# Kernel optimization log

Measured on AMD Instinct MI355X. Metric: run time of the kernel, lower is better.

## Reference

```python
import jax, jax.numpy as jnp
import numpy as np

B, N, DIM = 2, 128, 128
H, DH = 8, 32
DI = H * DH          # dim_inner = 256
DM = 2 * DI          # mlp_expansion_factor * dim_inner = 512
MAXDEG = 2
S = 1 + MAXDEG + MAXDEG  # 5
M1, M2 = 3, 5        # 2l+1 for degrees 1,2


def setup_inputs() -> dict:
    key = jax.random.key(0)
    ks = jax.random.split(key, 24)
    rn = lambda k, shp, sc=1.0: jax.random.normal(k, shp, jnp.float32) * sc
    s_d = DIM ** -0.5
    s_m = DM ** -0.5
    s_i = DI ** -0.5
    return {
        "h":    rn(ks[0], (B, N, DIM)),
        "t_ij": rn(ks[1], (B, N, N, DIM)),
        "r1":   rn(ks[2], (B, N, N, M1)),
        "r2":   rn(ks[3], (B, N, N, M2)),
        "x1":   rn(ks[4], (B, N, DIM, M1)),
        "x2":   rn(ks[5], (B, N, DIM, M2)),
        # LayerNorm gains (bias=False)
        "g_hi": jnp.ones((DIM,), jnp.float32),
        "g_hj": jnp.ones((DIM,), jnp.float32),
        # projections (stored as [in, out])
        "Wq":  rn(ks[6],  (DIM, DI), s_d),
        "Wk":  rn(ks[7],  (DIM, DI), s_d),
        "Wv1": rn(ks[8],  (DIM, DM), s_d), "bv1": jnp.zeros((DM,), jnp.float32),
        "Wv2": rn(ks[9],  (DM, S * DI), s_m), "bv2": jnp.zeros((S * DI,), jnp.float32),
        "Wpv1": rn(ks[10], (DIM, DM), s_d), "bpv1": jnp.zeros((DM,), jnp.float32),
        "Wpv2": rn(ks[11], (DM, S * DI), s_m), "bpv2": jnp.zeros((S * DI,), jnp.float32),
        "Wek": rn(ks[12], (DIM, S * DI), s_d),
        "Wev": rn(ks[13], (DIM, S * DI), s_d),
        "Wg":  rn(ks[14], (DIM, H * S), s_d), "bg": jnp.zeros((H * S,), jnp.float32),
        "Wo":  rn(ks[15], (DI, DIM), s_i),
    }


def _ln(x, g):
    mu = x.mean(-1, keepdims=True)
    var = ((x - mu) ** 2).mean(-1, keepdims=True)
    return (x - mu) / jnp.sqrt(var + 1e-5) * g


def reference(h, t_ij, r1, r2, x1, x2, g_hi, g_hj, Wq, Wk, Wv1, bv1, Wv2, bv2,
              Wpv1, bpv1, Wpv2, bpv2, Wek, Wev, Wg, bg, Wo):
    silu = jax.nn.silu
    hi = _ln(h, g_hi)  # b n d
    hj = _ln(h, g_hj)
    # queries/keys: b h n dh
    q = (hi @ Wq).reshape(B, N, H, DH).transpose(0, 2, 1, 3)
    k = (hj @ Wk).reshape(B, N, H, DH).transpose(0, 2, 1, 3)
    # node values / post-attn values: b h n s dh
    v  = (silu(hj @ Wv1 + bv1) @ Wv2 + bv2).reshape(B, N, S, H, DH).transpose(0, 3, 1, 2, 4)
    pv = (silu(hj @ Wpv1 + bpv1) @ Wpv2 + bpv2).reshape(B, N, S, H, DH).transpose(0, 3, 1, 2, 4)
    # edge keys/values: b h i j s dh
    ek = silu(t_ij @ Wek).reshape(B, N, N, S, H, DH).transpose(0, 4, 1, 2, 3, 5)
    ev = (t_ij @ Wev).reshape(B, N, N, S, H, DH).transpose(0, 4, 1, 2, 3, 5)
    # keys elementwise-conditioned by edge keys, then score over dh
    sim = jnp.einsum('bhid,bhjd,bhijsd->bhijs', q, k, ek)
    attn = jax.nn.softmax(sim, axis=3)  # softmax over j (dim=-2 of b h i j s)
    # sea_ij: b h i j s dh
    sea = attn[..., None] * v[:, :, None] + ev * pv[:, :, None]
    # gates: b h i 1 s 1
    gates = jax.nn.sigmoid(hi @ Wg + bg).reshape(B, N, H, S).transpose(0, 2, 1, 3)
    out = sea * gates[:, :, :, None, :, None]
    # merge heads -> b i j s (h dh), combine -> b i j s dim
    out = out.transpose(0, 2, 3, 4, 1, 5).reshape(B, N, N, S, DI) @ Wo
    # split along s: (1, maxdeg, maxdeg) = (h_scales, r_scales, x_scales)
    h_out = h + out[..., 0, :].sum(axis=2)  # sum over j
    x1_out = (jnp.einsum('bjdm,bijd->bidm', x1, out[..., 3, :])
              + jnp.einsum('bijm,bijd->bidm', r1, out[..., 1, :]))
    x2_out = (jnp.einsum('bjdm,bijd->bidm', x2, out[..., 4, :])
              + jnp.einsum('bijm,bijd->bidm', r2, out[..., 2, :]))
    return (h_out, x1_out, x2_out)
```

## Files before the change

### kernel.cpp

```cpp
#include <hip/hip_runtime.h>
#include <math.h>

#define BB 2
#define NN 128
#define DD 128
#define DI 256
#define DM 512
#define SS 5
#define SDI 1280
#define HS 40
#define M1 3
#define M2 5

typedef __attribute__((ext_vector_type(8))) short bf16x8_t;
typedef __attribute__((ext_vector_type(4))) float f32x4_t;
typedef __attribute__((ext_vector_type(4))) float f32x4v;

#define MFMA __builtin_amdgcn_mfma_f32_16x16x32_bf16

__device__ __forceinline__ float sigm(float x){ return __fdividef(1.0f, 1.0f + __expf(-x)); }
__device__ __forceinline__ unsigned short f2bf(float f){
    union { float f; unsigned u; } v; v.f = f;
    unsigned r = v.u + 0x7FFFu + ((v.u>>16)&1u);
    return (unsigned short)(r>>16);
}
__device__ __forceinline__ unsigned pk2(float a, float b){
    return (unsigned)f2bf(a) | ((unsigned)f2bf(b)<<16);
}
__device__ __forceinline__ float bflo(unsigned u){ union{unsigned u; float f;} v; v.u = u<<16; return v.f; }
__device__ __forceinline__ float bfhi(unsigned u){ union{unsigned u; float f;} v; v.u = u & 0xFFFF0000u; return v.f; }

__global__ __launch_bounds__(256) void prep(
    const float* __restrict__ h,
    const float* __restrict__ g_hi, const float* __restrict__ g_hj,
    const float* __restrict__ Wq, const float* __restrict__ Wk,
    const float* __restrict__ Wv1, const float* __restrict__ Wpv1,
    const float* __restrict__ Wg,
    const float* __restrict__ Wek, const float* __restrict__ Wev,
    const float* __restrict__ Wo, const float* __restrict__ Wv2,
    const float* __restrict__ Wpv2,
    const float* __restrict__ x1, const float* __restrict__ x2,
    unsigned short* __restrict__ hi_ws, unsigned short* __restrict__ hj_ws,
    unsigned short* __restrict__ WekT, unsigned short* __restrict__ WevT,
    unsigned short* __restrict__ WoT, unsigned short* __restrict__ W2T,
    unsigned short* __restrict__ WnT,
    float* __restrict__ x1T, float* __restrict__ x2T)
{
    const int bx = blockIdx.x, tid = threadIdx.x;
    __shared__ unsigned short sLT[64*65];
    if (bx < 408){
        const float* src; unsigned short* dst; int W, ldD, R0, C0;
        int t = bx;
        if (t < 160){ src=Wv2;  dst=W2T;            W=SDI; ldD=DM;  R0=(t%20)*64; C0=(t/20)*64; }
        else if (t < 320){ t-=160; src=Wpv2; dst=W2T + SDI*DM; W=SDI; ldD=DM; R0=(t%20)*64; C0=(t/20)*64; }
        else if (t < 360){ t-=320; src=Wek; dst=WekT; W=SDI; ldD=DD; R0=(t%20)*64; C0=(t/20)*64; }
        else if (t < 400){ t-=360; src=Wev; dst=WevT; W=SDI; ldD=DD; R0=(t%20)*64; C0=(t/20)*64; }
        else { t-=400; src=Wo; dst=WoT; W=DD; ldD=DI; R0=(t%2)*64; C0=(t/2)*64; }
        const int tx = tid & 63, ty = tid >> 6;
        #pragma unroll
        for (int k=0;k<16;++k){
            int c = C0 + 4*k + ty;
            sLT[tx*65 + 4*k + ty] = f2bf(src[(size_t)c*W + R0 + tx]);
        }
        __syncthreads();
        #pragma unroll
        for (int k=0;k<16;++k){
            int rr = 4*k + ty;
            dst[(size_t)(R0+rr)*ldD + C0 + tx] = sLT[rr*65 + tx];
        }
    } else if (bx < 664){
        const int node = bx - 408;
        if (tid < 64){
            float h0 = h[node*DD + tid], h1 = h[node*DD + 64 + tid];
            float s1 = h0 + h1, s2 = h0*h0 + h1*h1;
            #pragma unroll
            for (int off=32; off; off>>=1){ s1 += __shfl_xor(s1,off); s2 += __shfl_xor(s2,off); }
            float mu   = s1*(1.0f/DD);
            float var  = s2*(1.0f/DD) - mu*mu;
            float rstd = rsqrtf(var + 1e-5f);
            float c0 = (h0-mu)*rstd, c1 = (h1-mu)*rstd;
            hi_ws[node*DD + tid]      = f2bf(c0*g_hi[tid]);
            hi_ws[node*DD + 64 + tid] = f2bf(c1*g_hi[64+tid]);
            hj_ws[node*DD + tid]      = f2bf(c0*g_hj[tid]);
            hj_ws[node*DD + 64 + tid] = f2bf(c1*g_hj[64+tid]);
        }
        for (int f = node*256 + tid; f < 1584*DD; f += 256*256){
            int row = f >> 7, d = f & 127;
            float v;
            if (row < 256)       v = Wq[d*DI + row];
            else if (row < 304){ int c = row-256; v = (c < HS) ? Wg[d*HS + c] : 0.0f; }
            else if (row < 560)  v = Wk[d*DI + (row-304)];
            else if (row < 1072) v = Wv1[d*DM + (row-560)];
            else                 v = Wpv1[d*DM + (row-1072)];
            WnT[f] = f2bf(v);
        }
    } else {
        const int t = bx - 664;
        const int bb = t >> 7, j = t & 127;
        const int d = tid & 127, half = tid >> 7;
        if (half == 0){
            #pragma unroll
            for (int m=0;m<M1;++m)
                x1T[((size_t)(bb*M1+m)*NN + j)*DD + d] =
                    x1[(((size_t)bb*NN + j)*DD + d)*M1 + m];
        } else {
            #pragma unroll
            for (int m=0;m<M2;++m)
                x2T[((size_t)(bb*M2+m)*NN + j)*DD + d] =
                    x2[(((size_t)bb*NN + j)*DD + d)*M2 + m];
        }
    }
}

__global__ __launch_bounds__(256,4) void node_gemm(
    const unsigned short* __restrict__ WnT,
    const unsigned short* __restrict__ hi_ws, const unsigned short* __restrict__ hj_ws,
    const float* __restrict__ bg, const float* __restrict__ bv1, const float* __restrict__ bpv1,
    float* __restrict__ q_ws, float* __restrict__ k_ws,
    float* __restrict__ g_ws, unsigned short* __restrict__ hid_ws)
{
    const int bx = blockIdx.x;
    const int tile = bx % 99, nq = bx / 99;
    const int tid = threadIdx.x, lane = tid&63, w = tid>>6;
    const int l15 = lane&15, g4 = lane>>4;
    const int ntile = nq*4 + w;
    const unsigned short* A  = WnT + (size_t)(tile*16 + l15)*DD + 8*g4;
    const unsigned short* Bp = ((tile < 19) ? hi_ws : hj_ws) + (size_t)(ntile*16 + l15)*DD + 8*g4;
    f32x4_t c = {0.f,0.f,0.f,0.f};
    #pragma unroll
    for (int ks=0; ks<4; ++ks)
        c = MFMA(*(const bf16x8_t*)(A + 32*ks), *(const bf16x8_t*)(Bp + 32*ks), c, 0,0,0);
    const int node = ntile*16 + l15;
    const int col0 = tile*16 + 4*g4;
    if (tile < 16){
        f32x4_t* dst = (f32x4_t*)(q_ws + (size_t)node*DI + col0);
        *dst = c;
    } else if (tile < 19){
        #pragma unroll
        for (int r=0;r<4;++r){
            int cc = col0 + r - 256;
            if (cc < HS) g_ws[node*HS + cc] = sigm(c[r] + bg[cc]);
        }
    } else if (tile < 35){
        f32x4_t* dst = (f32x4_t*)(k_ws + (size_t)node*DI + (col0-304));
        *dst = c;
    } else if (tile < 67){
        int cc = col0 - 560;
        float s0 = c[0]+bv1[cc], s1 = c[1]+bv1[cc+1], s2 = c[2]+bv1[cc+2], s3 = c[3]+bv1[cc+3];
        s0 *= sigm(s0); s1 *= sigm(s1); s2 *= sigm(s2); s3 *= sigm(s3);
        uint2 pkk; pkk.x = pk2(s0,s1); pkk.y = pk2(s2,s3);
        *(uint2*)(hid_ws + (size_t)node*1024 + cc) = pkk;
    } else {
        int cc = col0 - 1072;
        float s0 = c[0]+bpv1[cc], s1 = c[1]+bpv1[cc+1], s2 = c[2]+bpv1[cc+2], s3 = c[3]+bpv1[cc+3];
        s0 *= sigm(s0); s1 *= sigm(s1); s2 *= sigm(s2); s3 *= sigm(s3);
        uint2 pkk; pkk.x = pk2(s0,s1); pkk.y = pk2(s2,s3);
        *(uint2*)(hid_ws + (size_t)node*1024 + 512 + cc) = pkk;
    }
}

__global__ __launch_bounds__(256,4) void v2_gemm(
    const unsigned short* __restrict__ W2T,
    const unsigned short* __restrict__ hid_ws,
    const float* __restrict__ bv2, const float* __restrict__ bpv2,
    unsigned short* __restrict__ vpv_ws)
{
    const int bx = blockIdx.x;
    const int otile = bx % 160, nq = bx / 160;
    const int tid = threadIdx.x, lane = tid&63, w = tid>>6;
    const int l15 = lane&15, g4 = lane>>4;
    const int ntile = nq*4 + w;
    const int obase = otile*16;
    const int koff = (obase < SDI) ? 0 : 512;
    const unsigned short* A  = W2T + (size_t)(obase + l15)*DM + 8*g4;
    const unsigned short* Bp = hid_ws + (size_t)(ntile*16 + l15)*1024 + koff + 8*g4;
    f32x4_t c = {0.f,0.f,0.f,0.f};
    #pragma unroll
    for (int ks=0; ks<16; ++ks)
        c = MFMA(*(const bf16x8_t*)(A + 32*ks), *(const bf16x8_t*)(Bp + 32*ks), c, 0,0,0);
    const int node = ntile*16 + l15;
    const int o0 = obase + 4*g4;
    const float* bias = (obase < SDI) ? bv2 : bpv2;
    const int ob = (obase < SDI) ? o0 : (o0 - SDI);
    float v0 = c[0]+bias[ob], v1 = c[1]+bias[ob+1], v2 = c[2]+bias[ob+2], v3 = c[3]+bias[ob+3];
    uint2 pkk; pkk.x = pk2(v0,v1); pkk.y = pk2(v2,v3);
    *(uint2*)(vpv_ws + (size_t)node*2560 + o0) = pkk;
}

#define SH_T   0
#define SH_QK  16384
#define SH_SIM 49152
#define SH_Q   59392

__global__ __launch_bounds__(512,4) void simh(
    const float* __restrict__ t_ij,
    const unsigned short* __restrict__ WekT,
    const float* __restrict__ q_ws, const float* __restrict__ k_ws,
    float* __restrict__ sim_ws)
{
    __shared__ __align__(16) char sm[60416];
    float* sSIM = (float*)(sm + SH_SIM);
    float* sQf  = (float*)(sm + SH_Q);

    const int bx0 = blockIdx.x;
    const int bx = ((bx0 & 7) << 6) | (bx0 >> 3);
    const int node = bx >> 1, jh = bx & 1;
    const int b = node >> 7;
    const int j0 = jh*64;
    const int tid = threadIdx.x, lane = tid&63, w = tid>>6;
    const int l15 = lane&15, g4 = lane>>4;

    if (tid < DI) sQf[tid] = q_ws[(size_t)node*DI + tid];
    {
        const int j = tid>>3, seg = tid&7;
        const float* src = t_ij + (size_t)(node*NN + j0 + j)*DD + seg*16;
        char* row = sm + SH_T + j*256;
        const int swz = (j&7)<<4;
        #pragma unroll
        for (int u=0;u<4;++u){
            f32x4v tv = __builtin_nontemporal_load((const f32x4v*)(src + 4*u));
            uint2 pkk; pkk.x = pk2(tv[0],tv[1]); pkk.y = pk2(tv[2],tv[3]);
            *(uint2*)(row + ((2*(seg*16+4*u)) ^ swz)) = pkk;
        }
    }
    __syncthreads();
    {
        const int j = tid>>3, seg = tid&7;
        const float* kr = k_ws + (size_t)(b*NN + j0 + j)*DI + seg*32;
        char* row = sm + SH_QK + j*512;
        const int swz = (j&7)<<4;
        #pragma unroll
        for (int u=0;u<8;++u){
            float4 kv = *(const float4*)(kr + 4*u);
            const float* qv = sQf + seg*32 + 4*u;
            uint2 pkk; pkk.x = pk2(kv.x*qv[0], kv.y*qv[1]); pkk.y = pk2(kv.z*qv[2], kv.w*qv[3]);
            *(uint2*)(row + ((2*(seg*32+4*u)) ^ swz)) = pkk;
        }
    }
    bf16x8_t bT[4][4];
    #pragma unroll
    for (int jt=0;jt<4;++jt){
        const int jc = jt*16 + l15;
        const char* row = sm + SH_T + jc*256;
        const int swz = (jc&7)<<4;
        #pragma unroll
        for (int ks=0;ks<4;++ks)
            bT[jt][ks] = *(const bf16x8_t*)(row + ((2*(32*ks+8*g4)) ^ swz));
    }
    __syncthreads();

    for (int p5=0; p5<5; ++p5){
        const int p = w + 8*p5;
        const unsigned short* ap = WekT + (size_t)(2*p)*16*DD + (size_t)l15*DD + 8*g4;
        bf16x8_t a0[4], a1[4];
        #pragma unroll
        for (int ks=0;ks<4;++ks){
            a0[ks] = *(const bf16x8_t*)(ap + 32*ks);
            a1[ks] = *(const bf16x8_t*)(ap + 16*DD + 32*ks);
        }
        const int hs = w*SS + p5;
        const int o0 = 32*p + 4*g4;
        const int qk0 = o0 & 255;
        #pragma unroll
        for (int jt=0;jt<4;++jt){
            f32x4_t c0 = {0.f,0.f,0.f,0.f}, c1 = {0.f,0.f,0.f,0.f};
            #pragma unroll
            for (int ks=0;ks<4;++ks){
                c0 = MFMA(a0[ks], bT[jt][ks], c0, 0,0,0);
                c1 = MFMA(a1[ks], bT[jt][ks], c1, 0,0,0);
            }
            const int jr = jt*16 + l15;
            const char* qrow = sm + SH_QK + jr*512;
            const int swz = (jr&7)<<4;
            uint2 u0 = *(const uint2*)(qrow + ((2*qk0) ^ swz));
            uint2 u1 = *(const uint2*)(qrow + ((2*(qk0+16)) ^ swz));
            float part =
                (c0[0]*sigm(c0[0]))*bflo(u0.x) + (c0[1]*sigm(c0[1]))*bfhi(u0.x)
              + (c0[2]*sigm(c0[2]))*bflo(u0.y) + (c0[3]*sigm(c0[3]))*bfhi(u0.y)
              + (c1[0]*sigm(c1[0]))*bflo(u1.x) + (c1[1]*sigm(c1[1]))*bfhi(u1.x)
              + (c1[2]*sigm(c1[2]))*bflo(u1.y) + (c1[3]*sigm(c1[3]))*bfhi(u1.y);
            part += __shfl_xor(part, 16);
            part += __shfl_xor(part, 32);
            if (g4 == 0) sSIM[jr*HS + hs] = part;
        }
    }
    __syncthreads();
    {
        float* dst = sim_ws + (size_t)node*NN*HS + j0*HS;
        for (int t2=tid; t2<64*HS; t2+=512) dst[t2] = sSIM[t2];
    }
}

__global__ __launch_bounds__(256) void softmax_k(
    float* __restrict__ sim_ws, const float* __restrict__ g_ws)
{
    const int node = blockIdx.x;
    const int tid = threadIdx.x, lane = tid&63, w = tid>>6;
    float* srow = sim_ws + (size_t)node*NN*HS;
    #pragma unroll
    for (int u=0; u<10; ++u){
        const int hs = w*10 + u;
        const float gt = g_ws[node*HS + hs];
        float v0 = srow[lane*HS + hs];
        float v1 = srow[(lane+64)*HS + hs];
        float m = fmaxf(v0,v1);
        #pragma unroll
        for (int off=32; off; off>>=1) m = fmaxf(m, __shfl_xor(m,off));
        float e0 = __expf(v0-m), e1 = __expf(v1-m);
        float ssum = e0+e1;
        #pragma unroll
        for (int off=32; off; off>>=1) ssum += __shfl_xor(ssum,off);
        float inv = __fdividef(gt, ssum);
        srow[lane*HS + hs]      = e0*inv;
        srow[(lane+64)*HS + hs] = e1*inv;
    }
}

#define EV_BODY(S, ATTIDX, EPILOG)                                                \
    _Pragma("unroll")                                                             \
    for (int mloc=0; mloc<2; ++mloc){                                             \
        const int mt = w*2 + mloc;                                                \
        const int m0 = mt*16 + 4*g4;                                              \
        uint2 vvr[4], ppr[4];                                                     \
        _Pragma("unroll")                                                         \
        for (int jt=0;jt<4;++jt){                                                 \
            const unsigned short* vb = vpv_ws + (size_t)(b*NN + j0 + jt*16 + l15)*2560 + (S)*DI + m0; \
            vvr[jt] = *(const uint2*)vb;                                          \
            ppr[jt] = *(const uint2*)(vb + SDI);                                  \
        }                                                                         \
        const unsigned short* ap = WevT + (size_t)((S)*DI + mt*16 + l15)*DD + 8*g4; \
        bf16x8_t aa[4];                                                           \
        _Pragma("unroll")                                                         \
        for (int ks=0;ks<4;++ks) aa[ks] = *(const bf16x8_t*)(ap + 32*ks);         \
        const int hh = mt >> 1;                                                   \
        const float gtv = sG[hh*SS + (S)];                                        \
        _Pragma("unroll")                                                         \
        for (int jt=0;jt<4;++jt){                                                 \
            const int jc = jt*16 + l15;                                           \
            bf16x8_t bT[4];                                                       \
            {   const char* row_ = sm + jc*256;                                   \
                const int swz_ = (jc&7)<<4;                                       \
                _Pragma("unroll")                                                 \
                for (int ks=0;ks<4;++ks)                                          \
                    bT[ks] = *(const bf16x8_t*)(row_ + ((2*(32*ks+8*g4)) ^ swz_)); } \
            f32x4_t c = {0.f,0.f,0.f,0.f};                                        \
            _Pragma("unroll")                                                     \
            for (int ks=0;ks<4;++ks) c = MFMA(aa[ks], bT[ks], c, 0,0,0);          \
            const float atv = sATT[ATTIDX];                                       \
            float g_[4];                                                          \
            g_[0] = atv*bflo(vvr[jt].x) + gtv*c[0]*bflo(ppr[jt].x);               \
            g_[1] = atv*bfhi(vvr[jt].x) + gtv*c[1]*bfhi(ppr[jt].x);               \
            g_[2] = atv*bflo(vvr[jt].y) + gtv*c[2]*bflo(ppr[jt].y);               \
            g_[3] = atv*bfhi(vvr[jt].y) + gtv*c[3]*bfhi(ppr[jt].y);               \
            EPILOG                                                                \
        }                                                                         \
    }

#define RED_WRITE(VAL, ROW, T_)                                                   \
    { float v_ = (VAL);                                                           \
      v_ += __shfl_xor(v_,1); v_ += __shfl_xor(v_,2);                             \
      v_ += __shfl_xor(v_,4); v_ += __shfl_xor(v_,8);                             \
      if (l15 == 0)                                                               \
          pdst[(ROW)*256 + (w*2 + ((T_)>>2))*16 + 4*g4 + ((T_)&3)] = v_; }

__global__ __launch_bounds__(512,4) void out_s012(
    const float* __restrict__ t_ij,
    const unsigned short* __restrict__ WevT,
    const unsigned short* __restrict__ vpv_ws,
    const float* __restrict__ attn_ws,
    const float* __restrict__ g_ws,
    const float* __restrict__ r1, const float* __restrict__ r2,
    float* __restrict__ p012)
{
    __shared__ __align__(16) char sm[24736];
    float* sATT = (float*)(sm + 16384);
    float* sG   = (float*)(sm + 22528);
    float* sW1  = (float*)(sm + 22688);
    float* sW2  = (float*)(sm + 23456);

    const int bx0 = blockIdx.x;
    const int bx = ((bx0 & 7) << 6) | (bx0 >> 3);
    const int node = bx >> 1, jh = bx & 1;
    const int b = node >> 7;
    const int j0 = jh*64;
    const int tid = threadIdx.x, lane = tid&63, w = tid>>6;
    const int l15 = lane&15, g4 = lane>>4;

    {
        const int j = tid>>3, seg = tid&7;
        const float* src = t_ij + (size_t)(node*NN + j0 + j)*DD + seg*16;
        char* row = sm + j*256;
        const int swz = (j&7)<<4;
        #pragma unroll
        for (int u=0;u<4;++u){
            f32x4v tv = __builtin_nontemporal_load((const f32x4v*)(src + 4*u));
            uint2 pkk; pkk.x = pk2(tv[0],tv[1]); pkk.y = pk2(tv[2],tv[3]);
            *(uint2*)(row + ((2*(seg*16+4*u)) ^ swz)) = pkk;
        }
    }
    {
        const float* asrc = attn_ws + (size_t)node*NN*HS + j0*HS;
        for (int t2=tid; t2<64*24; t2+=512){
            int j = t2/24, rem = t2 - 24*j, hh = rem/3, s = rem - 3*hh;
            sATT[t2] = asrc[j*HS + hh*SS + s];
        }
    }
    if (tid < HS) sG[tid] = g_ws[node*HS + tid];
    if (tid < 64*M1) sW1[tid] = r1[((size_t)node*NN + j0)*M1 + tid];
    if (tid < 64*M2) sW2[tid] = r2[((size_t)node*NN + j0)*M2 + tid];
    __syncthreads();

    float* pdst = p012 + (size_t)(jh*256 + node)*9*256;

    {
        float a0[8] = {0,0,0,0,0,0,0,0};
        EV_BODY(0, jc*24 + hh*3 + 0, {
            _Pragma("unroll")
            for (int k_=0;k_<4;++k_) a0[mloc*4+k_] += g_[k_];
        })
        #pragma unroll
        for (int t_=0;t_<8;++t_) RED_WRITE(a0[t_], 0, t_)
    }
    {
        float a1[M1][8];
        #pragma unroll
        for (int m_=0;m_<M1;++m_)
            #pragma unroll
            for (int t_=0;t_<8;++t_) a1[m_][t_] = 0.f;
        EV_BODY(1, jc*24 + hh*3 + 1, {
            _Pragma("unroll")
            for (int m_=0;m_<M1;++m_){
                const float wgt = sW1[jc*M1 + m_];
                _Pragma("unroll")
                for (int k_=0;k_<4;++k_) a1[m_][mloc*4+k_] = fmaf(wgt, g_[k_], a1[m_][mloc*4+k_]);
            }
        })
        #pragma unroll
        for (int m_=0;m_<M1;++m_)
            #pragma unroll
            for (int t_=0;t_<8;++t_) RED_WRITE(a1[m_][t_], 1+m_, t_)
    }
    {
        float a2[M2][8];
        #pragma unroll
        for (int m_=0;m_<M2;++m_)
            #pragma unroll
            for (int t_=0;t_<8;++t_) a2[m_][t_] = 0.f;
        EV_BODY(2, jc*24 + hh*3 + 2, {
            _Pragma("unroll")
            for (int m_=0;m_<M2;++m_){
                const float wgt = sW2[jc*M2 + m_];
                _Pragma("unroll")
                for (int k_=0;k_<4;++k_) a2[m_][mloc*4+k_] = fmaf(wgt, g_[k_], a2[m_][mloc*4+k_]);
            }
        })
        #pragma unroll
        for (int m_=0;m_<M2;++m_)
            #pragma unroll
            for (int t_=0;t_<8;++t_) RED_WRITE(a2[m_][t_], 4+m_, t_)
    }
}

#define O34_P  16384

#define P_WRITE34                                                                 \
    { uint2 pkk; pkk.x = pk2(g_[0],g_[1]); pkk.y = pk2(g_[2],g_[3]);              \
      *(uint2*)(sm + O34_P + jc*512 + ((2*m0) ^ ((jc&7)<<4))) = pkk; }

#define WO_X(XT, MM, AX)                                                          \
    _Pragma("unroll")                                                             \
    for (int jt=0; jt<4; ++jt){                                                   \
        float xv[4*(MM)];                                                         \
        _Pragma("unroll")                                                         \
        for (int r_=0;r_<4;++r_){                                                 \
            const int jr = j0 + jt*16 + 4*g4 + r_;                                \
            _Pragma("unroll")                                                     \
            for (int m_=0;m_<(MM);++m_)                                           \
                xv[r_*(MM)+m_] = XT[((size_t)(b*(MM)+m_)*NN + jr)*DD + d];        \
        }                                                                         \
        const int arow = jt*16 + l15;                                             \
        const char* pbp = sm + O34_P + arow*512;                                  \
        const int aswz = (arow&7)<<4;                                             \
        f32x4_t c = {0.f,0.f,0.f,0.f};                                            \
        _Pragma("unroll")                                                         \
        for (int ks=0;ks<8;++ks){                                                 \
            bf16x8_t a = *(const bf16x8_t*)(pbp + ((64*ks + 16*g4) ^ aswz));      \
            c = MFMA(a, bWo[ks], c, 0,0,0);                                       \
        }                                                                         \
        _Pragma("unroll")                                                         \
        for (int r_=0;r_<4;++r_){                                                 \
            _Pragma("unroll")                                                     \
            for (int m_=0;m_<(MM);++m_) AX[m_] = fmaf(xv[r_*(MM)+m_], c[r_], AX[m_]); \
        }                                                                         \
    }

__global__ __launch_bounds__(512,4) void out_s34(
    const float* __restrict__ t_ij,
    const unsigned short* __restrict__ WevT, const unsigned short* __restrict__ WoT,
    const unsigned short* __restrict__ vpv_ws,
    const float* __restrict__ attn_ws,
    const float* __restrict__ g_ws,
    const float* __restrict__ x1T, const float* __restrict__ x2T,
    float* __restrict__ p34)
{
    __shared__ __align__(16) char sm[53408];
    float* sATT = (float*)(sm + 49152);
    float* sG   = (float*)(sm + 53248);

    const int bx0 = blockIdx.x;
    const int bx = ((bx0 & 7) << 6) | (bx0 >> 3);
    const int node = bx >> 1, jh = bx & 1;
    const int b = node >> 7;
    const int j0 = jh*64;
    const int tid = threadIdx.x, lane = tid&63, w = tid>>6;
    const int l15 = lane&15, g4 = lane>>4;

    {
        const int j = tid>>3, seg = tid&7;
        const float* src = t_ij + (size_t)(node*NN + j0 + j)*DD + seg*16;
        char* row = sm + j*256;
        const int swz = (j&7)<<4;
        #pragma unroll
        for (int u=0;u<4;++u){
            f32x4v tv = __builtin_nontemporal_load((const f32x4v*)(src + 4*u));
            uint2 pkk; pkk.x = pk2(tv[0],tv[1]); pkk.y = pk2(tv[2],tv[3]);
            *(uint2*)(row + ((2*(seg*16+4*u)) ^ swz)) = pkk;
        }
    }
    {
        const float* asrc = attn_ws + (size_t)node*NN*HS + j0*HS;
        for (int t2=tid; t2<64*16; t2+=512){
            int j = t2>>4, rem = t2 & 15, hh = rem>>1, s = 3 + (rem&1);
            sATT[t2] = asrc[j*HS + hh*SS + s];
        }
    }
    if (tid < HS) sG[tid] = g_ws[node*HS + tid];
    bf16x8_t bWo[8];
    {
        const unsigned short* wr = WoT + (size_t)(w*16 + l15)*DI + 8*g4;
        #pragma unroll
        for (int ks=0;ks<8;++ks) bWo[ks] = *(const bf16x8_t*)(wr + 32*ks);
    }
    __syncthreads();

    const int d = w*16 + l15;
    float ax1[M1] = {0.f,0.f,0.f};
    float ax2[M2] = {0.f,0.f,0.f,0.f,0.f};

    EV_BODY(3, jc*16 + hh*2 + 0, P_WRITE34)
    __syncthreads();
    WO_X(x1T, M1, ax1)
    __syncthreads();
    EV_BODY(4, jc*16 + hh*2 + 1, P_WRITE34)
    __syncthreads();
    WO_X(x2T, M2, ax2)

    {
        float v0 = ax1[0], v1 = ax1[1], v2 = ax1[2];
        float v3 = ax2[0], v4 = ax2[1], v5 = ax2[2], v6 = ax2[3], v7 = ax2[4];
        v0 += __shfl_xor(v0,16); v0 += __shfl_xor(v0,32);
        v1 += __shfl_xor(v1,16); v1 += __shfl_xor(v1,32);
        v2 += __shfl_xor(v2,16); v2 += __shfl_xor(v2,32);
        v3 += __shfl_xor(v3,16); v3 += __shfl_xor(v3,32);
        v4 += __shfl_xor(v4,16); v4 += __shfl_xor(v4,32);
        v5 += __shfl_xor(v5,16); v5 += __shfl_xor(v5,32);
        v6 += __shfl_xor(v6,16); v6 += __shfl_xor(v6,32);
        v7 += __shfl_xor(v7,16); v7 += __shfl_xor(v7,32);
        if (g4 == 0){
            float* pb = p34 + (size_t)bx*8*DD + d;
            pb[0*DD] = v0; pb[1*DD] = v1; pb[2*DD] = v2;
            pb[3*DD] = v3; pb[4*DD] = v4; pb[5*DD] = v5;
            pb[6*DD] = v6; pb[7*DD] = v7;
        }
    }
}

__global__ __launch_bounds__(128) void combine(
    const float* __restrict__ h, const unsigned short* __restrict__ WoT,
    const float* __restrict__ p012, const float* __restrict__ p34,
    float* __restrict__ out_h, float* __restrict__ out_x1, float* __restrict__ out_x2)
{
    __shared__ float sZ[256*12];
    const int node = blockIdx.x, d = threadIdx.x;
    const float* pa = p012 + ((size_t)node*9)*256;
    const float* pb = p012 + ((size_t)(256 + node)*9)*256;
    for (int t=d; t<2304; t+=128){
        int m = t >> 8, c = t & 255;
        sZ[c*12 + m] = pa[t] + pb[t];
    }
    __syncthreads();
    float az[9] = {0.f,0.f,0.f,0.f,0.f,0.f,0.f,0.f,0.f};
    const unsigned short* wr = WoT + (size_t)d*DI;
    for (int cb=0; cb<32; ++cb){
        uint4 wv = *(const uint4*)(wr + cb*8);
        float wk[8];
        wk[0]=bflo(wv.x); wk[1]=bfhi(wv.x); wk[2]=bflo(wv.y); wk[3]=bfhi(wv.y);
        wk[4]=bflo(wv.z); wk[5]=bfhi(wv.z); wk[6]=bflo(wv.w); wk[7]=bfhi(wv.w);
        #pragma unroll
        for (int k=0;k<8;++k){
            const float* zb = sZ + (cb*8+k)*12;
            float4 za = *(const float4*)zb;
            float4 zbv = *(const float4*)(zb+4);
            float z8 = zb[8];
            az[0] = fmaf(za.x,  wk[k], az[0]);
            az[1] = fmaf(za.y,  wk[k], az[1]);
            az[2] = fmaf(za.z,  wk[k], az[2]);
            az[3] = fmaf(za.w,  wk[k], az[3]);
            az[4] = fmaf(zbv.x, wk[k], az[4]);
            az[5] = fmaf(zbv.y, wk[k], az[5]);
            az[6] = fmaf(zbv.z, wk[k], az[6]);
            az[7] = fmaf(zbv.w, wk[k], az[7]);
            az[8] = fmaf(z8,    wk[k], az[8]);
        }
    }
    float p34v[8];
    #pragma unroll
    for (int row=0; row<8; ++row){
        p34v[row] = p34[((size_t)(node*2+0)*8 + row)*DD + d]
                  + p34[((size_t)(node*2+1)*8 + row)*DD + d];
    }
    out_h[(size_t)node*DD + d] = h[(size_t)node*DD + d] + az[0];
    #pragma unroll
    for (int m=0;m<M1;++m)
        out_x1[((size_t)node*DD + d)*M1 + m] = az[1+m] + p34v[m];
    #pragma unroll
    for (int m=0;m<M2;++m)
        out_x2[((size_t)node*DD + d)*M2 + m] = az[4+m] + p34v[3+m];
}

extern "C" void kernel_launch(void* const* d_in, const int* in_sizes, int n_in,
                              void* d_out, int out_size, void* d_ws, size_t ws_size,
                              hipStream_t stream)
{
    (void)in_sizes; (void)n_in; (void)out_size; (void)ws_size;
    const float* h    = (const float*)d_in[0];
    const float* t_ij = (const float*)d_in[1];
    const float* r1   = (const float*)d_in[2];
    const float* r2   = (const float*)d_in[3];
    const float* x1   = (const float*)d_in[4];
    const float* x2   = (const float*)d_in[5];
    const float* g_hi = (const float*)d_in[6];
    const float* g_hj = (const float*)d_in[7];
    const float* Wq   = (const float*)d_in[8];
    const float* Wk   = (const float*)d_in[9];
    const float* Wv1  = (const float*)d_in[10];
    const float* bv1  = (const float*)d_in[11];
    const float* Wv2  = (const float*)d_in[12];
    const float* bv2  = (const float*)d_in[13];
    const float* Wpv1 = (const float*)d_in[14];
    const float* bpv1 = (const float*)d_in[15];
    const float* Wpv2 = (const float*)d_in[16];
    const float* bpv2 = (const float*)d_in[17];
    const float* Wek  = (const float*)d_in[18];
    const float* Wev  = (const float*)d_in[19];
    const float* Wg   = (const float*)d_in[20];
    const float* bg   = (const float*)d_in[21];
    const float* Wo   = (const float*)d_in[22];

    float* fb     = (float*)d_ws;
    float* q_ws   = fb;
    float* k_ws   = q_ws   + 65536;
    float* g_ws   = k_ws   + 65536;
    float* sim_ws = g_ws   + 10240;
    float* p012   = sim_ws + 1310720;
    float* p34    = p012   + 1179648;
    float* x1T    = p34    + 524288;
    float* x2T    = x1T    + 98304;
    unsigned short* hi_ws  = (unsigned short*)(x2T + 163840);
    unsigned short* hj_ws  = hi_ws  + 32768;
    unsigned short* hid_ws = hj_ws  + 32768;
    unsigned short* vpv_ws = hid_ws + 262144;
    unsigned short* WekT   = vpv_ws + 655360;
    unsigned short* WevT   = WekT   + 163840;
    unsigned short* WoT    = WevT   + 163840;
    unsigned short* W2T    = WoT    + 32768;
    unsigned short* WnT    = W2T    + 1310720;

    float* out_h  = (float*)d_out;
    float* out_x1 = out_h  + BB*NN*DD;
    float* out_x2 = out_x1 + BB*NN*DD*M1;

    prep<<<920, 256, 0, stream>>>(h, g_hi, g_hj, Wq, Wk, Wv1, Wpv1, Wg,
        Wek, Wev, Wo, Wv2, Wpv2, x1, x2,
        hi_ws, hj_ws, WekT, WevT, WoT, W2T, WnT, x1T, x2T);

    node_gemm<<<396, 256, 0, stream>>>(WnT, hi_ws, hj_ws, bg, bv1, bpv1,
        q_ws, k_ws, g_ws, hid_ws);

    v2_gemm<<<640, 256, 0, stream>>>(W2T, hid_ws, bv2, bpv2, vpv_ws);

    simh<<<512, 512, 0, stream>>>(t_ij, WekT, q_ws, k_ws, sim_ws);

    softmax_k<<<256, 256, 0, stream>>>(sim_ws, g_ws);

    out_s012<<<512, 512, 0, stream>>>(t_ij, WevT, vpv_ws, sim_ws, g_ws,
        r1, r2, p012);

    out_s34<<<512, 512, 0, stream>>>(t_ij, WevT, WoT, vpv_ws, sim_ws, g_ws,
        x1T, x2T, p34);

    combine<<<256, 128, 0, stream>>>(h, WoT, p012, p34, out_h, out_x1, out_x2);
}
```

Baseline: 182.3 us.

## Split j dimension into quarters for out_s012/out_s34 and store p012 partials as bf16

The two edge-output kernels now handle 32 j-rows per block instead of 64, which doubles the grid to 1024 blocks and halves shared memory per block, so more blocks can be resident at once. The partial sums p012 are written as bf16, and combine reduces over four partials instead of two. The goal is better occupancy and latency hiding in the heaviest kernels, at the cost of more partial-sum traffic, repeated per-block setup (weight loads), and lower precision in the p012 partials.

After: 196.2 us. 7.6% more time.

```diff
diff --git a/kernel.cpp b/kernel.cpp
--- a/kernel.cpp
+++ b/kernel.cpp
@@ -321,9 +321,9 @@
     for (int mloc=0; mloc<2; ++mloc){                                             \
         const int mt = w*2 + mloc;                                                \
         const int m0 = mt*16 + 4*g4;                                              \
-        uint2 vvr[4], ppr[4];                                                     \
+        uint2 vvr[2], ppr[2];                                                     \
         _Pragma("unroll")                                                         \
-        for (int jt=0;jt<4;++jt){                                                 \
+        for (int jt=0;jt<2;++jt){                                                 \
             const unsigned short* vb = vpv_ws + (size_t)(b*NN + j0 + jt*16 + l15)*2560 + (S)*DI + m0; \
             vvr[jt] = *(const uint2*)vb;                                          \
             ppr[jt] = *(const uint2*)(vb + SDI);                                  \
@@ -335,7 +335,7 @@
         const int hh = mt >> 1;                                                   \
         const float gtv = sG[hh*SS + (S)];                                        \
         _Pragma("unroll")                                                         \
-        for (int jt=0;jt<4;++jt){                                                 \
+        for (int jt=0;jt<2;++jt){                                                 \
             const int jc = jt*16 + l15;                                           \
             bf16x8_t bT[4];                                                       \
             {   const char* row_ = sm + jc*256;                                   \
@@ -361,7 +361,7 @@
       v_ += __shfl_xor(v_,1); v_ += __shfl_xor(v_,2);                             \
       v_ += __shfl_xor(v_,4); v_ += __shfl_xor(v_,8);                             \
       if (l15 == 0)                                                               \
-          pdst[(ROW)*256 + (w*2 + ((T_)>>2))*16 + 4*g4 + ((T_)&3)] = v_; }
+          pdst[(ROW)*256 + (w*2 + ((T_)>>2))*16 + 4*g4 + ((T_)&3)] = f2bf(v_); }
 
 __global__ __launch_bounds__(512,4) void out_s012(
     const float* __restrict__ t_ij,
@@ -370,47 +370,47 @@
     const float* __restrict__ attn_ws,
     const float* __restrict__ g_ws,
     const float* __restrict__ r1, const float* __restrict__ r2,
-    float* __restrict__ p012)
-{
-    __shared__ __align__(16) char sm[24736];
-    float* sATT = (float*)(sm + 16384);
-    float* sG   = (float*)(sm + 22528);
-    float* sW1  = (float*)(sm + 22688);
-    float* sW2  = (float*)(sm + 23456);
+    unsigned short* __restrict__ p012b)
+{
+    __shared__ __align__(16) char sm[12448];
+    float* sATT = (float*)(sm + 8192);
+    float* sG   = (float*)(sm + 11264);
+    float* sW1  = (float*)(sm + 11424);
+    float* sW2  = (float*)(sm + 11808);
 
     const int bx0 = blockIdx.x;
-    const int bx = ((bx0 & 7) << 6) | (bx0 >> 3);
-    const int node = bx >> 1, jh = bx & 1;
+    const int bx = ((bx0 & 7) << 7) | (bx0 >> 3);
+    const int node = bx >> 2, qt = bx & 3;
     const int b = node >> 7;
-    const int j0 = jh*64;
+    const int j0 = qt*32;
     const int tid = threadIdx.x, lane = tid&63, w = tid>>6;
     const int l15 = lane&15, g4 = lane>>4;
 
     {
-        const int j = tid>>3, seg = tid&7;
-        const float* src = t_ij + (size_t)(node*NN + j0 + j)*DD + seg*16;
+        const int j = tid>>4, seg = tid&15;
+        const float* src = t_ij + (size_t)(node*NN + j0 + j)*DD + seg*8;
         char* row = sm + j*256;
         const int swz = (j&7)<<4;
         #pragma unroll
-        for (int u=0;u<4;++u){
+        for (int u=0;u<2;++u){
             f32x4v tv = __builtin_nontemporal_load((const f32x4v*)(src + 4*u));
             uint2 pkk; pkk.x = pk2(tv[0],tv[1]); pkk.y = pk2(tv[2],tv[3]);
-            *(uint2*)(row + ((2*(seg*16+4*u)) ^ swz)) = pkk;
+            *(uint2*)(row + ((2*(seg*8+4*u)) ^ swz)) = pkk;
         }
     }
     {
         const float* asrc = attn_ws + (size_t)node*NN*HS + j0*HS;
-        for (int t2=tid; t2<64*24; t2+=512){
+        for (int t2=tid; t2<32*24; t2+=512){
             int j = t2/24, rem = t2 - 24*j, hh = rem/3, s = rem - 3*hh;
             sATT[t2] = asrc[j*HS + hh*SS + s];
         }
     }
     if (tid < HS) sG[tid] = g_ws[node*HS + tid];
-    if (tid < 64*M1) sW1[tid] = r1[((size_t)node*NN + j0)*M1 + tid];
-    if (tid < 64*M2) sW2[tid] = r2[((size_t)node*NN + j0)*M2 + tid];
-    __syncthreads();
-
-    float* pdst = p012 + (size_t)(jh*256 + node)*9*256;
+    if (tid < 32*M1) sW1[tid] = r1[((size_t)node*NN + j0)*M1 + tid];
+    if (tid < 32*M2) sW2[tid] = r2[((size_t)node*NN + j0)*M2 + tid];
+    __syncthreads();
+
+    unsigned short* pdst = p012b + (size_t)(qt*256 + node)*9*256;
 
     {
         float a0[8] = {0,0,0,0,0,0,0,0};
@@ -461,7 +461,7 @@
     }
 }
 
-#define O34_P  16384
+#define O34_P  8192
 
 #define P_WRITE34                                                                 \
     { uint2 pkk; pkk.x = pk2(g_[0],g_[1]); pkk.y = pk2(g_[2],g_[3]);              \
@@ -469,7 +469,7 @@
 
 #define WO_X(XT, MM, AX)                                                          \
     _Pragma("unroll")                                                             \
-    for (int jt=0; jt<4; ++jt){                                                   \
+    for (int jt=0; jt<2; ++jt){                                                   \
         float xv[4*(MM)];                                                         \
         _Pragma("unroll")                                                         \
         for (int r_=0;r_<4;++r_){                                                 \
@@ -503,36 +503,34 @@
     const float* __restrict__ x1T, const float* __restrict__ x2T,
     float* __restrict__ p34)
 {
-    __shared__ __align__(16) char sm[53408];
-    float* sATT = (float*)(sm + 49152);
-    float* sG   = (float*)(sm + 53248);
+    __shared__ __align__(16) char sm[26784];
+    float* sATT = (float*)(sm + 24576);
+    float* sG   = (float*)(sm + 26624);
 
     const int bx0 = blockIdx.x;
-    const int bx = ((bx0 & 7) << 6) | (bx0 >> 3);
-    const int node = bx >> 1, jh = bx & 1;
+    const int bx = ((bx0 & 7) << 7) | (bx0 >> 3);
+    const int node = bx >> 2, qt = bx & 3;
     const int b = node >> 7;
-    const int j0 = jh*64;
+    const int j0 = qt*32;
     const int tid = threadIdx.x, lane = tid&63, w = tid>>6;
     const int l15 = lane&15, g4 = lane>>4;
 
     {
-        const int j = tid>>3, seg = tid&7;
-        const float* src = t_ij + (size_t)(node*NN + j0 + j)*DD + seg*16;
+        const int j = tid>>4, seg = tid&15;
+        const float* src = t_ij + (size_t)(node*NN + j0 + j)*DD + seg*8;
         char* row = sm + j*256;
         const int swz = (j&7)<<4;
         #pragma unroll
-        for (int u=0;u<4;++u){
+        for (int u=0;u<2;++u){
             f32x4v tv = __builtin_nontemporal_load((const f32x4v*)(src + 4*u));
             uint2 pkk; pkk.x = pk2(tv[0],tv[1]); pkk.y = pk2(tv[2],tv[3]);
-            *(uint2*)(row + ((2*(seg*16+4*u)) ^ swz)) = pkk;
-        }
-    }
-    {
+            *(uint2*)(row + ((2*(seg*8+4*u)) ^ swz)) = pkk;
+        }
+    }
+    if (tid < 32*16){
         const float* asrc = attn_ws + (size_t)node*NN*HS + j0*HS;
-        for (int t2=tid; t2<64*16; t2+=512){
-            int j = t2>>4, rem = t2 & 15, hh = rem>>1, s = 3 + (rem&1);
-            sATT[t2] = asrc[j*HS + hh*SS + s];
-        }
+        int j = tid>>4, rem = tid & 15, hh = rem>>1, s = 3 + (rem&1);
+        sATT[tid] = asrc[j*HS + hh*SS + s];
     }
     if (tid < HS) sG[tid] = g_ws[node*HS + tid];
     bf16x8_t bWo[8];
@@ -577,16 +575,18 @@
 
 __global__ __launch_bounds__(128) void combine(
     const float* __restrict__ h, const unsigned short* __restrict__ WoT,
-    const float* __restrict__ p012, const float* __restrict__ p34,
+    const unsigned short* __restrict__ p012b, const float* __restrict__ p34,
     float* __restrict__ out_h, float* __restrict__ out_x1, float* __restrict__ out_x2)
 {
     __shared__ float sZ[256*12];
     const int node = blockIdx.x, d = threadIdx.x;
-    const float* pa = p012 + ((size_t)node*9)*256;
-    const float* pb = p012 + ((size_t)(256 + node)*9)*256;
     for (int t=d; t<2304; t+=128){
         int m = t >> 8, c = t & 255;
-        sZ[c*12 + m] = pa[t] + pb[t];
+        float s = 0.f;
+        #pragma unroll
+        for (int q=0;q<4;++q)
+            s += bflo((unsigned)p012b[((size_t)(q*256 + node)*9)*256 + t]);
+        sZ[c*12 + m] = s;
     }
     __syncthreads();
     float az[9] = {0.f,0.f,0.f,0.f,0.f,0.f,0.f,0.f,0.f};
@@ -616,8 +616,11 @@
     float p34v[8];
     #pragma unroll
     for (int row=0; row<8; ++row){
-        p34v[row] = p34[((size_t)(node*2+0)*8 + row)*DD + d]
-                  + p34[((size_t)(node*2+1)*8 + row)*DD + d];
+        float s = 0.f;
+        #pragma unroll
+        for (int q=0;q<4;++q)
+            s += p34[((size_t)(node*4+q)*8 + row)*DD + d];
+        p34v[row] = s;
     }
     out_h[(size_t)node*DD + d] = h[(size_t)node*DD + d] + az[0];
     #pragma unroll
@@ -662,11 +665,11 @@
     float* k_ws   = q_ws   + 65536;
     float* g_ws   = k_ws   + 65536;
     float* sim_ws = g_ws   + 10240;
-    float* p012   = sim_ws + 1310720;
-    float* p34    = p012   + 1179648;
-    float* x1T    = p34    + 524288;
+    float* p34    = sim_ws + 1310720;
+    float* x1T    = p34    + 1048576;
     float* x2T    = x1T    + 98304;
-    unsigned short* hi_ws  = (unsigned short*)(x2T + 163840);
+    unsigned short* p012b  = (unsigned short*)(x2T + 163840);
+    unsigned short* hi_ws  = p012b  + 2359296;
     unsigned short* hj_ws  = hi_ws  + 32768;
     unsigned short* hid_ws = hj_ws  + 32768;
     unsigned short* vpv_ws = hid_ws + 262144;
@@ -693,11 +696,11 @@
 
     softmax_k<<<256, 256, 0, stream>>>(sim_ws, g_ws);
 
-    out_s012<<<512, 512, 0, stream>>>(t_ij, WevT, vpv_ws, sim_ws, g_ws,
-        r1, r2, p012);
-
-    out_s34<<<512, 512, 0, stream>>>(t_ij, WevT, WoT, vpv_ws, sim_ws, g_ws,
+    out_s012<<<1024, 512, 0, stream>>>(t_ij, WevT, vpv_ws, sim_ws, g_ws,
+        r1, r2, p012b);
+
+    out_s34<<<1024, 512, 0, stream>>>(t_ij, WevT, WoT, vpv_ws, sim_ws, g_ws,
         x1T, x2T, p34);
 
-    combine<<<256, 128, 0, stream>>>(h, WoT, p012, p34, out_h, out_x1, out_x2);
-}
+    combine<<<256, 128, 0, stream>>>(h, WoT, p012b, p34, out_h, out_x1, out_x2);
+}
```
